# Kernel tuning notes

Measured on AMD Instinct MI355X. Metric: run time of the kernel, lower is better.

The kernel has to match this reference:

```python
import jax, jax.numpy as jnp
import numpy as np
import math

D_MODEL = 1024
N_HEADS = 16
D_K = D_MODEL // N_HEADS
HIDDEN = 4096
R_SOFTPLUS_0 = 1.442695041
EPS = 1e-6


def setup_inputs() -> dict:
    key = jax.random.key(0)
    ks = jax.random.split(key, 16)
    B, S = 4, 2048
    s = 0.02
    inp = {
        "inputs": jax.random.normal(ks[0], (B, S, D_MODEL), jnp.float32),
        "mask": jnp.zeros((1, 1, S, S), jnp.float32),
        # RmsNorm (direct_scale=True -> init 1.0)
        "rms_scale": jnp.ones((D_MODEL,), jnp.float32),
        # attention projections (torch Linear: y = x @ W.T + b)
        "Wq": jax.random.normal(ks[1], (D_MODEL, D_MODEL), jnp.float32) * s,
        "bq": jnp.zeros((D_MODEL,), jnp.float32),
        "Wk": jax.random.normal(ks[2], (D_MODEL, D_MODEL), jnp.float32) * s,
        "bk": jnp.zeros((D_MODEL,), jnp.float32),
        "Wv": jax.random.normal(ks[3], (D_MODEL, D_MODEL), jnp.float32) * s,
        "bv": jnp.zeros((D_MODEL,), jnp.float32),
        "per_dim_scale": jnp.zeros((D_K,), jnp.float32),
        "Wpost": jax.random.normal(ks[4], (D_MODEL, D_MODEL), jnp.float32) * s,
        "bpost": jnp.zeros((D_MODEL,), jnp.float32),
        # FFN LayerNorm (direct_scale=False -> scale param init 0, effective 1+scale)
        "ln_scale": jnp.zeros((D_MODEL,), jnp.float32),
        "ln_bias": jnp.zeros((D_MODEL,), jnp.float32),
        "W1": jax.random.normal(ks[5], (HIDDEN, D_MODEL), jnp.float32) * s,
        "b1": jnp.zeros((HIDDEN,), jnp.float32),
        "W2": jax.random.normal(ks[6], (D_MODEL, HIDDEN), jnp.float32) * s,
        "b2": jnp.zeros((D_MODEL,), jnp.float32),
    }
    return inp


def _rms_norm(x, scale):
    ms = jnp.mean(x * x, axis=-1, keepdims=True)
    return x * jax.lax.rsqrt(ms + EPS) * scale


def _layer_norm(x, scale, bias):
    mean = jnp.mean(x, axis=-1, keepdims=True)
    var = jnp.mean((x - mean) ** 2, axis=-1, keepdims=True)
    return (x - mean) * jax.lax.rsqrt(var + EPS) * (1.0 + scale) + bias


def reference(inputs, mask, rms_scale, Wq, bq, Wk, bk, Wv, bv, per_dim_scale,
              Wpost, bpost, ln_scale, ln_bias, W1, b1, W2, b2):
    B, S, _ = inputs.shape
    x = _rms_norm(inputs, rms_scale)
    # projections -> [B, H, S, Dk]
    def split_heads(t):
        return t.reshape(B, S, N_HEADS, D_K).transpose(0, 2, 1, 3)
    q = split_heads(x @ Wq.T + bq)
    k = split_heads(x @ Wk.T + bk)
    v = split_heads(x @ Wv.T + bv)
    # PerDimScale: (r_softplus_0 / sqrt(d_k)) * softplus(param)
    scale = (R_SOFTPLUS_0 / math.sqrt(D_K)) * jax.nn.softplus(per_dim_scale)
    q = q * scale
    attn = jnp.einsum("bhqd,bhkd->bhqk", q, k) + mask
    attn = jax.nn.softmax(attn, axis=-1)
    out = jnp.einsum("bhqk,bhkd->bhqd", attn, v)
    out = out.transpose(0, 2, 1, 3).reshape(B, S, D_MODEL)
    attn_out = out @ Wpost.T + bpost
    h = attn_out + inputs  # residual (dropout=0)
    # FeedForward with pre-LayerNorm and residual
    y = _layer_norm(h, ln_scale, ln_bias)
    y = jax.nn.relu(y @ W1.T + b1)
    y = y @ W2.T + b2
    return y + h
```

## Files before the change

kernel.cpp:

```cpp
#include <hip/hip_runtime.h>
#include <hip/hip_bf16.h>

typedef unsigned short u16;
typedef __attribute__((ext_vector_type(8))) short short8;
typedef __attribute__((ext_vector_type(4))) float floatx4;

#define R_PDS 0.18033688f
#define LOG2E 1.4426950408889634f

__device__ __forceinline__ float bf2f(u16 u) {
    union { float f; unsigned int i; } c; c.i = ((unsigned int)u) << 16; return c.f;
}
__device__ __forceinline__ u16 f2b(float f) {
    union { float f; unsigned int i; } c; c.f = f;
    unsigned int r = c.i + 0x7fffu + ((c.i >> 16) & 1u);
    return (u16)(r >> 16);
}
__device__ __forceinline__ unsigned int pk2(float a, float b) {
    __hip_bfloat162 h = __float22bfloat162_rn(float2{a, b});
    unsigned int u; __builtin_memcpy(&u, &h, 4); return u;
}

__device__ __forceinline__ void async16(const u16* g, u16* l) {
    __builtin_amdgcn_global_load_lds(
        (const __attribute__((address_space(1))) unsigned int*)g,
        (__attribute__((address_space(3))) unsigned int*)l, 16, 0, 0);
}

__global__ __launch_bounds__(256) void f2b_all_k(const float* __restrict__ Wq, const float* __restrict__ Wk,
                                                 const float* __restrict__ Wv, const float* __restrict__ Wp,
                                                 const float* __restrict__ W1, const float* __restrict__ W2,
                                                 u16* __restrict__ Wqkvb, u16* __restrict__ Wpb,
                                                 u16* __restrict__ W1b,  u16* __restrict__ W2b,
                                                 int* flag) {
    int bid = blockIdx.x;
    if (bid == 0 && threadIdx.x == 0) *flag = 0;
    const float* src; u16* dst; int off;
    if      (bid < 1024) { src = Wq; dst = Wqkvb;                off = bid; }
    else if (bid < 2048) { src = Wk; dst = Wqkvb + 1024 * 1024;  off = bid - 1024; }
    else if (bid < 3072) { src = Wv; dst = Wqkvb + 2048 * 1024;  off = bid - 2048; }
    else if (bid < 4096) { src = Wp; dst = Wpb;                  off = bid - 3072; }
    else if (bid < 8192) { src = W1; dst = W1b;                  off = bid - 4096; }
    else                 { src = W2; dst = W2b;                  off = bid - 8192; }
    int i = off * 256 + threadIdx.x;
    float4 v = ((const float4*)src)[i];
    uint2 w; w.x = pk2(v.x, v.y); w.y = pk2(v.z, v.w);
    ((uint2*)dst)[i] = w;
}

__global__ __launch_bounds__(256) void mask_any_k(const float* __restrict__ mask, int* flag) {
    int i = blockIdx.x * 256 + threadIdx.x;
    uint4 u = ((const uint4*)mask)[i];
    unsigned int v = (u.x | u.y | u.z | u.w) & 0x7fffffffu;
    if (v) atomicOr(flag, 1);
}

__global__ __launch_bounds__(256) void rmsnorm_k(const float* __restrict__ in,
                                                 const float* __restrict__ gscale,
                                                 u16* __restrict__ out) {
    int row = blockIdx.x;
    int t = threadIdx.x, lane = t & 63, wave = t >> 6;
    const float* x = in + (size_t)row * 1024;
    float4 v = *(const float4*)(x + t * 4);
    float ss = v.x*v.x + v.y*v.y + v.z*v.z + v.w*v.w;
    for (int o = 1; o < 64; o <<= 1) ss += __shfl_xor(ss, o, 64);
    __shared__ float red[4];
    if (lane == 0) red[wave] = ss;
    __syncthreads();
    float tot = red[0] + red[1] + red[2] + red[3];
    float inv = rsqrtf(tot * (1.0f / 1024.0f) + 1e-6f);
    float4 s = *(const float4*)(gscale + t * 4);
    uint2 w;
    w.x = pk2(v.x * inv * s.x, v.y * inv * s.y);
    w.y = pk2(v.z * inv * s.z, v.w * inv * s.w);
    *(uint2*)(out + (size_t)row * 1024 + t * 4) = w;
}

__global__ __launch_bounds__(256) void layernorm_k(const u16* __restrict__ in,
                                                   const float* __restrict__ gs,
                                                   const float* __restrict__ gb,
                                                   u16* __restrict__ out) {
    int row = blockIdx.x;
    int t = threadIdx.x, lane = t & 63, wave = t >> 6;
    const u16* x = in + (size_t)row * 1024;
    uint2 u = *(const uint2*)(x + t * 4);
    float v0 = bf2f((u16)(u.x & 0xffff)), v1 = bf2f((u16)(u.x >> 16));
    float v2 = bf2f((u16)(u.y & 0xffff)), v3 = bf2f((u16)(u.y >> 16));
    float s1 = v0 + v1 + v2 + v3;
    float s2 = v0*v0 + v1*v1 + v2*v2 + v3*v3;
    for (int o = 1; o < 64; o <<= 1) { s1 += __shfl_xor(s1, o, 64); s2 += __shfl_xor(s2, o, 64); }
    __shared__ float r1[4], r2[4];
    if (lane == 0) { r1[wave] = s1; r2[wave] = s2; }
    __syncthreads();
    float mean = (r1[0] + r1[1] + r1[2] + r1[3]) * (1.0f / 1024.0f);
    float var  = (r2[0] + r2[1] + r2[2] + r2[3]) * (1.0f / 1024.0f) - mean * mean;
    var = fmaxf(var, 0.0f);
    float inv = rsqrtf(var + 1e-6f);
    float4 sc = *(const float4*)(gs + t * 4);
    float4 bb = *(const float4*)(gb + t * 4);
    uint2 w;
    w.x = pk2((v0 - mean) * inv * (1.0f + sc.x) + bb.x,
              (v1 - mean) * inv * (1.0f + sc.y) + bb.y);
    w.y = pk2((v2 - mean) * inv * (1.0f + sc.z) + bb.z,
              (v3 - mean) * inv * (1.0f + sc.w) + bb.w);
    *(uint2*)(out + (size_t)row * 1024 + t * 4) = w;
}

__device__ __forceinline__ void xcd_swizzle(int& bx, int& by) {
    int gx = gridDim.x, nwg = gx * gridDim.y;
    int lin = blockIdx.y * gx + blockIdx.x;
    int swz = (lin & 7) * (nwg >> 3) + (lin >> 3);
    bx = swz % gx; by = swz / gx;
}

__device__ __forceinline__ void gemm8_core(const u16* __restrict__ A, const u16* __restrict__ B,
                                           int K, int NG, int m0, int n0,
                                           u16* lds, floatx4 (&acc)[8][4]) {
    const int t = threadIdx.x, wave = t >> 6, lane = t & 63;
    const int quad = lane >> 4, ln = lane & 15;
    const int wave_m = wave >> 2, wave_n = wave & 3;

    const int rowS = t >> 3;
    const int srcb = ((t & 7) * 16) ^ (((t >> 3) & 7) << 4);
    const u16* Ab = A + (size_t)(m0 + rowS) * K + (srcb >> 1);
    const u16* Bb = B + (size_t)(n0 + rowS) * K + (srcb >> 1);
    const size_t rstep = (size_t)64 * K;
    const size_t hstep = (size_t)128 * K;
    const int ldw = wave * 512;

    #define STAGE_A8(buf, h, kt) do { \
        u16* _l = lds + (buf) * 32768 + (h) * 8192 + ldw; \
        const u16* _g = Ab + (size_t)(h) * hstep + (kt); \
        async16(_g, _l); async16(_g + rstep, _l + 4096); } while (0)
    #define STAGE_B8(buf, h, kt) do { \
        u16* _l = lds + (buf) * 32768 + 16384 + (h) * 8192 + ldw; \
        const u16* _g = Bb + (size_t)(h) * hstep + (kt); \
        async16(_g, _l); async16(_g + rstep, _l + 4096); } while (0)

    #define RD8(base, lr, ks) \
        (*(const short8*)((base) + (lr) * 64 + ((((ks) * 64 + quad * 16) ^ (((lr) & 7) << 4)) >> 1)))

    STAGE_B8(0, 0, 0); STAGE_B8(0, 1, 0);
    STAGE_A8(0, 0, 0); STAGE_A8(0, 1, 0);
    if (NG > 1) {
        STAGE_B8(1, 0, 64); STAGE_B8(1, 1, 64);
        asm volatile("s_waitcnt vmcnt(4)" ::: "memory");
    } else {
        asm volatile("s_waitcnt vmcnt(0)" ::: "memory");
    }
    __builtin_amdgcn_s_barrier();

    for (int g = 0; g < NG; ++g) {
        const int cur = g & 1;
        const u16* aH = lds + cur * 32768 + wave_m * 8192;
        const u16* bH = lds + cur * 32768 + 16384 + (wave_n >> 1) * 8192;
        const int lrB = (wave_n & 1) * 64;
        short8 bf[4][2];
        #pragma unroll
        for (int q = 0; q < 4; ++q) {
            short8 af[2][2];
            #pragma unroll
            for (int mt = 0; mt < 2; ++mt)
                #pragma unroll
                for (int ks = 0; ks < 2; ++ks)
                    af[mt][ks] = RD8(aH, q * 32 + mt * 16 + ln, ks);
            if (q == 0) {
                #pragma unroll
                for (int nt = 0; nt < 4; ++nt)
                    #pragma unroll
                    for (int ks = 0; ks < 2; ++ks)
                        bf[nt][ks] = RD8(bH, lrB + nt * 16 + ln, ks);
            }
            if (q == 0 && g + 1 < NG) STAGE_A8(cur ^ 1, 0, (g + 1) * 64);
            if (q == 1 && g + 1 < NG) STAGE_A8(cur ^ 1, 1, (g + 1) * 64);
            if (q == 2 && g + 2 < NG) STAGE_B8(cur, 0, (g + 2) * 64);
            if (q == 3 && g + 2 < NG) STAGE_B8(cur, 1, (g + 2) * 64);
            __builtin_amdgcn_s_barrier();
            asm volatile("s_waitcnt lgkmcnt(0)" ::: "memory");
            __builtin_amdgcn_sched_barrier(0);
            __builtin_amdgcn_s_setprio(1);
            #pragma unroll
            for (int ks = 0; ks < 2; ++ks)
                #pragma unroll
                for (int mt = 0; mt < 2; ++mt)
                    #pragma unroll
                    for (int nt = 0; nt < 4; ++nt)
                        acc[q * 2 + mt][nt] = __builtin_amdgcn_mfma_f32_16x16x32_bf16(
                            af[mt][ks], bf[nt][ks], acc[q * 2 + mt][nt], 0, 0, 0);
            __builtin_amdgcn_s_setprio(0);
            __builtin_amdgcn_sched_barrier(0);
            if (q == 3 && g + 1 < NG) {
                if (g + 2 < NG) asm volatile("s_waitcnt vmcnt(4)" ::: "memory");
                else            asm volatile("s_waitcnt vmcnt(0)" ::: "memory");
            }
            __builtin_amdgcn_s_barrier();
        }
    }
    #undef STAGE_A8
    #undef STAGE_B8
    #undef RD8
}

__device__ __forceinline__ void gemm8h_core(const u16* __restrict__ A, const u16* __restrict__ B,
                                            int K, int NG, int m0, int n0,
                                            u16* lds, floatx4 (&acc)[4][4]) {
    const int t = threadIdx.x, wave = t >> 6, lane = t & 63;
    const int quad = lane >> 4, ln = lane & 15;
    const int wm = (wave >> 2) * 64, wn = (wave & 3) * 64;

    const int rowS = t >> 3;
    const int srcb = ((t & 7) * 16) ^ (((t >> 3) & 7) << 4);
    const u16* Ab = A + (size_t)(m0 + rowS) * K + (srcb >> 1);
    const u16* Bb = B + (size_t)(n0 + rowS) * K + (srcb >> 1);
    const size_t hstep = (size_t)64 * K;
    const int ldw = wave * 512;

    #define STAGE_AH(buf, h, kt) \
        async16(Ab + (size_t)(h) * hstep + (kt), lds + (buf) * 24576 + (h) * 4096 + ldw)
    #define STAGE_BH(buf, h, kt) \
        async16(Bb + (size_t)(h) * hstep + (kt), lds + (buf) * 24576 + 8192 + (h) * 4096 + ldw)
    #define RD8H(base, lr, ks) \
        (*(const short8*)((base) + (lr) * 64 + ((((ks) * 64 + quad * 16) ^ (((lr) & 7) << 4)) >> 1)))

    STAGE_BH(0, 0, 0); STAGE_BH(0, 1, 0); STAGE_BH(0, 2, 0); STAGE_BH(0, 3, 0);
    STAGE_AH(0, 0, 0); STAGE_AH(0, 1, 0);
    if (NG > 1) {
        STAGE_BH(1, 0, 64); STAGE_BH(1, 1, 64); STAGE_BH(1, 2, 64); STAGE_BH(1, 3, 64);
        asm volatile("s_waitcnt vmcnt(4)" ::: "memory");
    } else {
        asm volatile("s_waitcnt vmcnt(0)" ::: "memory");
    }
    __builtin_amdgcn_s_barrier();

    for (int g = 0; g < NG; ++g) {
        const int cur = g & 1;
        const u16* aB = lds + cur * 24576;
        const u16* bB = lds + cur * 24576 + 8192;
        short8 bf[4][2];
        #pragma unroll
        for (int q = 0; q < 2; ++q) {
            short8 af[2][2];
            #pragma unroll
            for (int mt = 0; mt < 2; ++mt)
                #pragma unroll
                for (int ks = 0; ks < 2; ++ks)
                    af[mt][ks] = RD8H(aB, wm + (q * 2 + mt) * 16 + ln, ks);
            if (q == 0) {
                #pragma unroll
                for (int nt = 0; nt < 4; ++nt)
                    #pragma unroll
                    for (int ks = 0; ks < 2; ++ks)
                        bf[nt][ks] = RD8H(bB, wn + nt * 16 + ln, ks);
            }
            if (q == 0 && g + 1 < NG) {
                STAGE_AH(cur ^ 1, 0, (g + 1) * 64); STAGE_AH(cur ^ 1, 1, (g + 1) * 64);
            }
            if (q == 1 && g + 2 < NG) {
                STAGE_BH(cur, 0, (g + 2) * 64); STAGE_BH(cur, 1, (g + 2) * 64);
                STAGE_BH(cur, 2, (g + 2) * 64); STAGE_BH(cur, 3, (g + 2) * 64);
            }
            __builtin_amdgcn_s_barrier();
            asm volatile("s_waitcnt lgkmcnt(0)" ::: "memory");
            __builtin_amdgcn_sched_barrier(0);
            __builtin_amdgcn_s_setprio(1);
            #pragma unroll
            for (int ks = 0; ks < 2; ++ks)
                #pragma unroll
                for (int mt = 0; mt < 2; ++mt)
                    #pragma unroll
                    for (int nt = 0; nt < 4; ++nt)
                        acc[q * 2 + mt][nt] = __builtin_amdgcn_mfma_f32_16x16x32_bf16(
                            af[mt][ks], bf[nt][ks], acc[q * 2 + mt][nt], 0, 0, 0);
            __builtin_amdgcn_s_setprio(0);
            __builtin_amdgcn_sched_barrier(0);
            if (q == 1 && g + 1 < NG) {
                if (g + 2 < NG) asm volatile("s_waitcnt vmcnt(4)" ::: "memory");
                else            asm volatile("s_waitcnt vmcnt(0)" ::: "memory");
            }
            __builtin_amdgcn_s_barrier();
        }
    }
    #undef STAGE_AH
    #undef STAGE_BH
    #undef RD8H
}

template <int EPI, bool OUTF32, bool RESF32>
__global__ __launch_bounds__(512, 2) void gemm8_bt_k(const u16* __restrict__ A,
                                                     const u16* __restrict__ B,
                                                     const float* __restrict__ bias,
                                                     const void* __restrict__ res,
                                                     void* __restrict__ Cv,
                                                     int M, int N, int K) {
    __shared__ __align__(16) u16 lds[65536];
    int bx, by; xcd_swizzle(bx, by);
    const int m0 = by * 256, n0 = bx * 256;
    const int t = threadIdx.x, wave = t >> 6, lane = t & 63;
    const int quad = lane >> 4, ln = lane & 15;
    const int wm = (wave >> 2) * 128, wn = (wave & 3) * 64;

    floatx4 acc[8][4];
    #pragma unroll
    for (int mf = 0; mf < 8; mf++)
        #pragma unroll
        for (int nf = 0; nf < 4; nf++) acc[mf][nf] = (floatx4)0.0f;

    gemm8_core(A, B, K, K >> 6, m0, n0, lds, acc);

    #pragma unroll
    for (int nf = 0; nf < 4; nf++) {
        int col = n0 + wn + nf * 16 + ln;
        float bv = bias[col];
        #pragma unroll
        for (int mf = 0; mf < 8; mf++) {
            int row = m0 + wm + mf * 16 + quad * 4;
            #pragma unroll
            for (int r = 0; r < 4; r++) {
                float v = acc[mf][nf][r] + bv;
                if (EPI == 1) v = fmaxf(v, 0.0f);
                if (EPI == 2) {
                    if (RESF32) v += ((const float*)res)[(size_t)(row + r) * N + col];
                    else        v += bf2f(((const u16*)res)[(size_t)(row + r) * N + col]);
                }
                if (OUTF32) ((float*)Cv)[(size_t)(row + r) * N + col] = v;
                else        ((u16*)Cv)[(size_t)(row + r) * N + col] = f2b(v);
            }
        }
    }
}

template <int EPI, bool OUTF32, bool RESF32>
__global__ __launch_bounds__(512, 2) void gemm8h_bt_k(const u16* __restrict__ A,
                                                      const u16* __restrict__ B,
                                                      const float* __restrict__ bias,
                                                      const void* __restrict__ res,
                                                      void* __restrict__ Cv,
                                                      int M, int N, int K) {
    __shared__ __align__(16) u16 lds[49152];
    int bx, by; xcd_swizzle(bx, by);
    const int m0 = by * 128, n0 = bx * 256;
    const int t = threadIdx.x, wave = t >> 6, lane = t & 63;
    const int quad = lane >> 4, ln = lane & 15;
    const int wm = (wave >> 2) * 64, wn = (wave & 3) * 64;

    floatx4 acc[4][4];
    #pragma unroll
    for (int mf = 0; mf < 4; mf++)
        #pragma unroll
        for (int nf = 0; nf < 4; nf++) acc[mf][nf] = (floatx4)0.0f;

    gemm8h_core(A, B, K, K >> 6, m0, n0, lds, acc);

    #pragma unroll
    for (int nf = 0; nf < 4; nf++) {
        int col = n0 + wn + nf * 16 + ln;
        float bv = bias[col];
        #pragma unroll
        for (int mf = 0; mf < 4; mf++) {
            int row = m0 + wm + mf * 16 + quad * 4;
            #pragma unroll
            for (int r = 0; r < 4; r++) {
                float v = acc[mf][nf][r] + bv;
                if (EPI == 1) v = fmaxf(v, 0.0f);
                if (EPI == 2) {
                    if (RESF32) v += ((const float*)res)[(size_t)(row + r) * N + col];
                    else        v += bf2f(((const u16*)res)[(size_t)(row + r) * N + col]);
                }
                if (OUTF32) ((float*)Cv)[(size_t)(row + r) * N + col] = v;
                else        ((u16*)Cv)[(size_t)(row + r) * N + col] = f2b(v);
            }
        }
    }
}

__global__ __launch_bounds__(512, 2) void gemm8h_qkv_k(const u16* __restrict__ A,
                                                       const u16* __restrict__ B,
                                                       const float* __restrict__ bq,
                                                       const float* __restrict__ bk,
                                                       const float* __restrict__ bv,
                                                       const float* __restrict__ pds,
                                                       u16* __restrict__ C) {
    const int K = 1024, N = 3072;
    __shared__ __align__(16) u16 lds[49152];
    int bx, by; xcd_swizzle(bx, by);
    const int m0 = by * 128, n0 = bx * 256;
    const int t = threadIdx.x, wave = t >> 6, lane = t & 63;
    const int quad = lane >> 4, ln = lane & 15;
    const int wm = (wave >> 2) * 64, wn = (wave & 3) * 64;

    floatx4 acc[4][4];
    #pragma unroll
    for (int mf = 0; mf < 4; mf++)
        #pragma unroll
        for (int nf = 0; nf < 4; nf++) acc[mf][nf] = (floatx4)0.0f;

    gemm8h_core(A, B, K, K >> 6, m0, n0, lds, acc);

    #pragma unroll
    for (int nf = 0; nf < 4; nf++) {
        int col = n0 + wn + nf * 16 + ln;
        float bv_, sc = 1.0f;
        if (col < 1024) {
            bv_ = bq[col];
            float xp = pds[col & 63];
            float sp = (xp > 20.0f) ? xp : log1pf(__expf(xp));
            sc = R_PDS * sp * LOG2E;
        } else if (col < 2048) bv_ = bk[col - 1024];
        else                   bv_ = bv[col - 2048];
        #pragma unroll
        for (int mf = 0; mf < 4; mf++) {
            int row = m0 + wm + mf * 16 + quad * 4;
            #pragma unroll
            for (int r = 0; r < 4; r++)
                C[(size_t)(row + r) * N + col] = f2b((acc[mf][nf][r] + bv_) * sc);
        }
    }
}

__global__ __launch_bounds__(256) void transpose_v_k(const u16* __restrict__ qkv, u16* __restrict__ vT) {
    __shared__ u16 tile[64][65];
    int st = blockIdx.x, bh = blockIdx.y;
    int b = bh >> 4, h = bh & 15;
    const u16* vb = qkv + (size_t)(b * 2048 + st * 64) * 3072 + 2048 + h * 64;
    int t = threadIdx.x;
    for (int i = t; i < 4096; i += 256) {
        int s = i >> 6, d = i & 63;
        tile[s][d] = vb[(size_t)s * 3072 + d];
    }
    __syncthreads();
    u16* ob = vT + (size_t)bh * 131072 + st * 64;
    for (int i = t; i < 4096; i += 256) {
        int d = i >> 6, s = i & 63;
        ob[(size_t)d * 2048 + s] = tile[s][d];
    }
}

__global__ __launch_bounds__(256) void attn_k(const u16* __restrict__ qkv,
                                              const u16* __restrict__ vT,
                                              const float* __restrict__ mask,
                                              const int* __restrict__ flag,
                                              u16* __restrict__ o) {
    __shared__ __align__(16) u16 QPs[128][72];
    __shared__ __align__(16) u16 Ks[64][72];
    __shared__ __align__(16) u16 Vs[64][72];

    const int t = threadIdx.x, wave = t >> 6, lane = t & 63;
    const int quad = lane >> 4, ln = lane & 15;
    const int qt = blockIdx.x, bh = blockIdx.y;
    const int b = bh >> 4, h = bh & 15;
    const int q0 = qt * 128;
    const int wm = wave * 32;

    const u16* qb = qkv + (size_t)(b * 2048 + q0) * 3072 + h * 64;
    for (int c = t; c < 1024; c += 256) {
        int row = c >> 3, seg = c & 7;
        *(uint4*)&QPs[row][seg * 8] = *(const uint4*)(qb + (size_t)row * 3072 + seg * 8);
    }
    __syncthreads();

    short8 qf[2][2];
    for (int mt = 0; mt < 2; mt++)
        for (int ks = 0; ks < 2; ks++)
            qf[mt][ks] = *(const short8*)&QPs[wm + mt * 16 + ln][ks * 32 + quad * 8];

    short8 ones_f;
    for (int i = 0; i < 8; i++) ones_f[i] = (short)0x3F80;

    floatx4 acc_o[2][4], acc_l[2];
    for (int mt = 0; mt < 2; mt++) {
        acc_l[mt] = (floatx4)0.0f;
        for (int dt = 0; dt < 4; dt++) acc_o[mt][dt] = (floatx4)0.0f;
    }

    const int mflag = *flag;
    const u16* kb = qkv + (size_t)(b * 2048) * 3072 + 1024 + h * 64;
    const u16* vg = vT + (size_t)bh * 131072;

    const int r0 = t >> 3, s0 = (t & 7) * 8;
    const u16* kp0 = kb + (size_t)r0 * 3072 + s0;
    const u16* kp1 = kb + (size_t)(r0 + 32) * 3072 + s0;
    const u16* vp0 = vg + (size_t)r0 * 2048 + s0;
    const u16* vp1 = vg + (size_t)(r0 + 32) * 2048 + s0;

    uint4 kr0 = *(const uint4*)(kp0);
    uint4 kr1 = *(const uint4*)(kp1);
    uint4 vr0 = *(const uint4*)(vp0);
    uint4 vr1 = *(const uint4*)(vp1);

    for (int kv0 = 0; kv0 < 2048; kv0 += 64) {
        __syncthreads();
        *(uint4*)&Ks[r0][s0]      = kr0;
        *(uint4*)&Ks[r0 + 32][s0] = kr1;
        *(uint4*)&Vs[r0][s0]      = vr0;
        *(uint4*)&Vs[r0 + 32][s0] = vr1;
        __syncthreads();
        if (kv0 + 64 < 2048) {
            size_t ko = (size_t)(kv0 + 64) * 3072;
            int    vo = kv0 + 64;
            kr0 = *(const uint4*)(kp0 + ko);
            kr1 = *(const uint4*)(kp1 + ko);
            vr0 = *(const uint4*)(vp0 + vo);
            vr1 = *(const uint4*)(vp1 + vo);
        }

        for (int nt = 0; nt < 4; nt++) {
            floatx4 sa0 = (floatx4)0.0f, sa1 = (floatx4)0.0f;
            for (int ks = 0; ks < 2; ks++) {
                short8 kf = *(const short8*)&Ks[nt * 16 + ln][ks * 32 + quad * 8];
                sa0 = __builtin_amdgcn_mfma_f32_16x16x32_bf16(kf, qf[0][ks], sa0, 0, 0, 0);
                sa1 = __builtin_amdgcn_mfma_f32_16x16x32_bf16(kf, qf[1][ks], sa1, 0, 0, 0);
            }
            if (mflag) {
                for (int r = 0; r < 4; r++) {
                    int kc = kv0 + nt * 16 + quad * 4 + r;
                    sa0[r] += mask[(size_t)(q0 + wm + ln) * 2048 + kc] * LOG2E;
                    sa1[r] += mask[(size_t)(q0 + wm + 16 + ln) * 2048 + kc] * LOG2E;
                }
            }
            {
                uint2 w;
                w.x = pk2(__builtin_amdgcn_exp2f(fminf(sa0[0], 80.0f)),
                          __builtin_amdgcn_exp2f(fminf(sa0[1], 80.0f)));
                w.y = pk2(__builtin_amdgcn_exp2f(fminf(sa0[2], 80.0f)),
                          __builtin_amdgcn_exp2f(fminf(sa0[3], 80.0f)));
                *(uint2*)&QPs[wm + ln][nt * 16 + quad * 4] = w;
            }
            {
                uint2 w;
                w.x = pk2(__builtin_amdgcn_exp2f(fminf(sa1[0], 80.0f)),
                          __builtin_amdgcn_exp2f(fminf(sa1[1], 80.0f)));
                w.y = pk2(__builtin_amdgcn_exp2f(fminf(sa1[2], 80.0f)),
                          __builtin_amdgcn_exp2f(fminf(sa1[3], 80.0f)));
                *(uint2*)&QPs[wm + 16 + ln][nt * 16 + quad * 4] = w;
            }
        }

        for (int ks = 0; ks < 2; ks++) {
            short8 a0 = *(const short8*)&QPs[wm + ln][ks * 32 + quad * 8];
            short8 a1 = *(const short8*)&QPs[wm + 16 + ln][ks * 32 + quad * 8];
            acc_l[0] = __builtin_amdgcn_mfma_f32_16x16x32_bf16(a0, ones_f, acc_l[0], 0, 0, 0);
            acc_l[1] = __builtin_amdgcn_mfma_f32_16x16x32_bf16(a1, ones_f, acc_l[1], 0, 0, 0);
            for (int dt = 0; dt < 4; dt++) {
                short8 bfr = *(const short8*)&Vs[dt * 16 + ln][ks * 32 + quad * 8];
                acc_o[0][dt] = __builtin_amdgcn_mfma_f32_16x16x32_bf16(a0, bfr, acc_o[0][dt], 0, 0, 0);
                acc_o[1][dt] = __builtin_amdgcn_mfma_f32_16x16x32_bf16(a1, bfr, acc_o[1][dt], 0, 0, 0);
            }
        }
    }

    u16* ob = o + (size_t)(b * 2048 + q0) * 1024 + h * 64;
    for (int mt = 0; mt < 2; mt++) {
        for (int r = 0; r < 4; r++) {
            float inv = 1.0f / acc_l[mt][r];
            int row = wm + mt * 16 + quad * 4 + r;
            for (int dt = 0; dt < 4; dt++)
                ob[(size_t)row * 1024 + dt * 16 + ln] = f2b(acc_o[mt][dt][r] * inv);
        }
    }
}

extern "C" void kernel_launch(void* const* d_in, const int* in_sizes, int n_in,
                              void* d_out, int out_size, void* d_ws, size_t ws_size,
                              hipStream_t stream) {
    const float* inp    = (const float*)d_in[0];
    const float* mask   = (const float*)d_in[1];
    const float* rms_s  = (const float*)d_in[2];
    const float* Wq     = (const float*)d_in[3];
    const float* bq     = (const float*)d_in[4];
    const float* Wk     = (const float*)d_in[5];
    const float* bk     = (const float*)d_in[6];
    const float* Wv     = (const float*)d_in[7];
    const float* bv     = (const float*)d_in[8];
    const float* pds    = (const float*)d_in[9];
    const float* Wpost  = (const float*)d_in[10];
    const float* bpost  = (const float*)d_in[11];
    const float* ln_s   = (const float*)d_in[12];
    const float* ln_b   = (const float*)d_in[13];
    const float* W1     = (const float*)d_in[14];
    const float* b1     = (const float*)d_in[15];
    const float* W2     = (const float*)d_in[16];
    const float* b2     = (const float*)d_in[17];
    float* out = (float*)d_out;

    char* w = (char*)d_ws;
    const size_t MB = 1u << 20;
    u16* W1b   = (u16*)(w + 0 * MB);
    u16* W2b   = (u16*)(w + 8 * MB);
    u16* qkv   = (u16*)(w + 16 * MB);
    u16* x     = (u16*)(w + 64 * MB);
    u16* o     = (u16*)(w + 64 * MB);
    u16* Wqkvb = (u16*)(w + 80 * MB);
    u16* Wpb   = (u16*)(w + 86 * MB);
    u16* yln   = (u16*)(w + 80 * MB);
    u16* vT    = (u16*)(w + 96 * MB);
    u16* hb    = (u16*)(w + 96 * MB);
    u16* f1    = (u16*)(w + 16 * MB);
    int* flag  = (int*)(w + 112 * MB);

    f2b_all_k<<<12288, 256, 0, stream>>>(Wq, Wk, Wv, Wpost, W1, W2, Wqkvb, Wpb, W1b, W2b, flag);
    mask_any_k<<<4096, 256, 0, stream>>>(mask, flag);

    rmsnorm_k<<<8192, 256, 0, stream>>>(inp, rms_s, x);

    gemm8h_qkv_k<<<dim3(12, 64), 512, 0, stream>>>(x, Wqkvb, bq, bk, bv, pds, qkv);

    transpose_v_k<<<dim3(32, 64), 256, 0, stream>>>(qkv, vT);

    attn_k<<<dim3(16, 64), 256, 0, stream>>>(qkv, vT, mask, flag, o);

    gemm8h_bt_k<2, false, true><<<dim3(4, 64), 512, 0, stream>>>(o, Wpb, bpost, inp, hb, 8192, 1024, 1024);

    layernorm_k<<<8192, 256, 0, stream>>>(hb, ln_s, ln_b, yln);

    gemm8_bt_k<1, false, true><<<dim3(16, 32), 512, 0, stream>>>(yln, W1b, b1, nullptr, f1, 8192, 4096, 1024);
    gemm8h_bt_k<2, true, false><<<dim3(4, 64), 512, 0, stream>>>(f1, W2b, b2, hb, out, 8192, 1024, 4096);
}
```

Baseline: 556.9 us.

## Enlarge attention query tile to 256 rows with swizzled LDS and remapped blocks

The attention kernel now processes 256 query rows per block instead of 128, with each wave owning four 16-row M tiles. Each K/V tile loaded into LDS therefore feeds twice as many MFMAs. LDS padding is replaced by an XOR swizzle to avoid bank conflicts with denser storage. Block indices are remapped so neighbouring blocks share a head, for L2 locality. The cost is more accumulator registers (launch bounds ask for 2 blocks per SM) and half as many blocks, which may lower occupancy.

Measured after the change: 506.2 us. -9.1%, faster.

```diff
diff --git a/kernel.cpp b/kernel.cpp
--- a/kernel.cpp
+++ b/kernel.cpp
@@ -435,40 +435,53 @@
     }
 }
 
-__global__ __launch_bounds__(256) void attn_k(const u16* __restrict__ qkv,
-                                              const u16* __restrict__ vT,
-                                              const float* __restrict__ mask,
-                                              const int* __restrict__ flag,
-                                              u16* __restrict__ o) {
-    __shared__ __align__(16) u16 QPs[128][72];
-    __shared__ __align__(16) u16 Ks[64][72];
-    __shared__ __align__(16) u16 Vs[64][72];
+__global__ __launch_bounds__(256, 2) void attn_k(const u16* __restrict__ qkv,
+                                                 const u16* __restrict__ vT,
+                                                 const float* __restrict__ mask,
+                                                 const int* __restrict__ flag,
+                                                 u16* __restrict__ o) {
+    __shared__ __align__(16) u16 QPs[256 * 64];
+    __shared__ __align__(16) u16 Ks[64 * 64];
+    __shared__ __align__(16) u16 Vs[64 * 64];
 
     const int t = threadIdx.x, wave = t >> 6, lane = t & 63;
     const int quad = lane >> 4, ln = lane & 15;
-    const int qt = blockIdx.x, bh = blockIdx.y;
+    const int lin = blockIdx.y * 8 + blockIdx.x;
+    const int qt = (lin >> 3) & 7;
+    const int bh = ((lin & 7) << 3) | (lin >> 6);
     const int b = bh >> 4, h = bh & 15;
-    const int q0 = qt * 128;
-    const int wm = wave * 32;
+    const int q0 = qt * 256;
+    const int wm = wave * 64;
 
     const u16* qb = qkv + (size_t)(b * 2048 + q0) * 3072 + h * 64;
-    for (int c = t; c < 1024; c += 256) {
+    #pragma unroll
+    for (int i = 0; i < 8; i++) {
+        int c = t + i * 256;
         int row = c >> 3, seg = c & 7;
-        *(uint4*)&QPs[row][seg * 8] = *(const uint4*)(qb + (size_t)row * 3072 + seg * 8);
+        int byt = (seg * 16) ^ ((row & 7) << 4);
+        *(uint4*)&QPs[row * 64 + (byt >> 1)] = *(const uint4*)(qb + (size_t)row * 3072 + seg * 8);
     }
     __syncthreads();
 
-    short8 qf[2][2];
-    for (int mt = 0; mt < 2; mt++)
-        for (int ks = 0; ks < 2; ks++)
-            qf[mt][ks] = *(const short8*)&QPs[wm + mt * 16 + ln][ks * 32 + quad * 8];
+    short8 qf[4][2];
+    #pragma unroll
+    for (int mt = 0; mt < 4; mt++)
+        #pragma unroll
+        for (int ks = 0; ks < 2; ks++) {
+            int row = wm + mt * 16 + ln;
+            int byt = (ks * 64 + quad * 16) ^ ((ln & 7) << 4);
+            qf[mt][ks] = *(const short8*)&QPs[row * 64 + (byt >> 1)];
+        }
 
     short8 ones_f;
+    #pragma unroll
     for (int i = 0; i < 8; i++) ones_f[i] = (short)0x3F80;
 
-    floatx4 acc_o[2][4], acc_l[2];
-    for (int mt = 0; mt < 2; mt++) {
+    floatx4 acc_o[4][4], acc_l[4];
+    #pragma unroll
+    for (int mt = 0; mt < 4; mt++) {
         acc_l[mt] = (floatx4)0.0f;
+        #pragma unroll
         for (int dt = 0; dt < 4; dt++) acc_o[mt][dt] = (floatx4)0.0f;
     }
 
@@ -476,7 +489,9 @@
     const u16* kb = qkv + (size_t)(b * 2048) * 3072 + 1024 + h * 64;
     const u16* vg = vT + (size_t)bh * 131072;
 
-    const int r0 = t >> 3, s0 = (t & 7) * 8;
+    const int r0 = t >> 3, sseg = t & 7;
+    const int wofs = (((sseg * 16) ^ ((r0 & 7) << 4)) >> 1);
+    const int s0 = sseg * 8;
     const u16* kp0 = kb + (size_t)r0 * 3072 + s0;
     const u16* kp1 = kb + (size_t)(r0 + 32) * 3072 + s0;
     const u16* vp0 = vg + (size_t)r0 * 2048 + s0;
@@ -489,10 +504,10 @@
 
     for (int kv0 = 0; kv0 < 2048; kv0 += 64) {
         __syncthreads();
-        *(uint4*)&Ks[r0][s0]      = kr0;
-        *(uint4*)&Ks[r0 + 32][s0] = kr1;
-        *(uint4*)&Vs[r0][s0]      = vr0;
-        *(uint4*)&Vs[r0 + 32][s0] = vr1;
+        *(uint4*)&Ks[r0 * 64 + wofs]        = kr0;
+        *(uint4*)&Ks[(r0 + 32) * 64 + wofs] = kr1;
+        *(uint4*)&Vs[r0 * 64 + wofs]        = vr0;
+        *(uint4*)&Vs[(r0 + 32) * 64 + wofs] = vr1;
         __syncthreads();
         if (kv0 + 64 < 2048) {
             size_t ko = (size_t)(kv0 + 64) * 3072;
@@ -503,56 +518,72 @@
             vr1 = *(const uint4*)(vp1 + vo);
         }
 
+        #pragma unroll
         for (int nt = 0; nt < 4; nt++) {
-            floatx4 sa0 = (floatx4)0.0f, sa1 = (floatx4)0.0f;
+            floatx4 sa[4];
+            #pragma unroll
+            for (int mt = 0; mt < 4; mt++) sa[mt] = (floatx4)0.0f;
+            #pragma unroll
             for (int ks = 0; ks < 2; ks++) {
-                short8 kf = *(const short8*)&Ks[nt * 16 + ln][ks * 32 + quad * 8];
-                sa0 = __builtin_amdgcn_mfma_f32_16x16x32_bf16(kf, qf[0][ks], sa0, 0, 0, 0);
-                sa1 = __builtin_amdgcn_mfma_f32_16x16x32_bf16(kf, qf[1][ks], sa1, 0, 0, 0);
+                int byt = (ks * 64 + quad * 16) ^ ((ln & 7) << 4);
+                short8 kf = *(const short8*)&Ks[(nt * 16 + ln) * 64 + (byt >> 1)];
+                #pragma unroll
+                for (int mt = 0; mt < 4; mt++)
+                    sa[mt] = __builtin_amdgcn_mfma_f32_16x16x32_bf16(kf, qf[mt][ks], sa[mt], 0, 0, 0);
             }
             if (mflag) {
-                for (int r = 0; r < 4; r++) {
-                    int kc = kv0 + nt * 16 + quad * 4 + r;
-                    sa0[r] += mask[(size_t)(q0 + wm + ln) * 2048 + kc] * LOG2E;
-                    sa1[r] += mask[(size_t)(q0 + wm + 16 + ln) * 2048 + kc] * LOG2E;
-                }
-            }
-            {
+                #pragma unroll
+                for (int mt = 0; mt < 4; mt++)
+                    #pragma unroll
+                    for (int r = 0; r < 4; r++) {
+                        int kc = kv0 + nt * 16 + quad * 4 + r;
+                        sa[mt][r] += mask[(size_t)(q0 + wm + mt * 16 + ln) * 2048 + kc] * LOG2E;
+                    }
+            }
+            #pragma unroll
+            for (int mt = 0; mt < 4; mt++) {
                 uint2 w;
-                w.x = pk2(__builtin_amdgcn_exp2f(fminf(sa0[0], 80.0f)),
-                          __builtin_amdgcn_exp2f(fminf(sa0[1], 80.0f)));
-                w.y = pk2(__builtin_amdgcn_exp2f(fminf(sa0[2], 80.0f)),
-                          __builtin_amdgcn_exp2f(fminf(sa0[3], 80.0f)));
-                *(uint2*)&QPs[wm + ln][nt * 16 + quad * 4] = w;
-            }
-            {
-                uint2 w;
-                w.x = pk2(__builtin_amdgcn_exp2f(fminf(sa1[0], 80.0f)),
-                          __builtin_amdgcn_exp2f(fminf(sa1[1], 80.0f)));
-                w.y = pk2(__builtin_amdgcn_exp2f(fminf(sa1[2], 80.0f)),
-                          __builtin_amdgcn_exp2f(fminf(sa1[3], 80.0f)));
-                *(uint2*)&QPs[wm + 16 + ln][nt * 16 + quad * 4] = w;
-            }
-        }
-
+                w.x = pk2(__builtin_amdgcn_exp2f(fminf(sa[mt][0], 80.0f)),
+                          __builtin_amdgcn_exp2f(fminf(sa[mt][1], 80.0f)));
+                w.y = pk2(__builtin_amdgcn_exp2f(fminf(sa[mt][2], 80.0f)),
+                          __builtin_amdgcn_exp2f(fminf(sa[mt][3], 80.0f)));
+                int row = wm + mt * 16 + ln;
+                int byt = (nt * 32 + quad * 8) ^ ((ln & 7) << 4);
+                *(uint2*)&QPs[row * 64 + (byt >> 1)] = w;
+            }
+        }
+
+        #pragma unroll
         for (int ks = 0; ks < 2; ks++) {
-            short8 a0 = *(const short8*)&QPs[wm + ln][ks * 32 + quad * 8];
-            short8 a1 = *(const short8*)&QPs[wm + 16 + ln][ks * 32 + quad * 8];
-            acc_l[0] = __builtin_amdgcn_mfma_f32_16x16x32_bf16(a0, ones_f, acc_l[0], 0, 0, 0);
-            acc_l[1] = __builtin_amdgcn_mfma_f32_16x16x32_bf16(a1, ones_f, acc_l[1], 0, 0, 0);
+            short8 a[4];
+            #pragma unroll
+            for (int mt = 0; mt < 4; mt++) {
+                int row = wm + mt * 16 + ln;
+                int byt = (ks * 64 + quad * 16) ^ ((ln & 7) << 4);
+                a[mt] = *(const short8*)&QPs[row * 64 + (byt >> 1)];
+            }
+            #pragma unroll
+            for (int mt = 0; mt < 4; mt++)
+                acc_l[mt] = __builtin_amdgcn_mfma_f32_16x16x32_bf16(a[mt], ones_f, acc_l[mt], 0, 0, 0);
+            #pragma unroll
             for (int dt = 0; dt < 4; dt++) {
-                short8 bfr = *(const short8*)&Vs[dt * 16 + ln][ks * 32 + quad * 8];
-                acc_o[0][dt] = __builtin_amdgcn_mfma_f32_16x16x32_bf16(a0, bfr, acc_o[0][dt], 0, 0, 0);
-                acc_o[1][dt] = __builtin_amdgcn_mfma_f32_16x16x32_bf16(a1, bfr, acc_o[1][dt], 0, 0, 0);
+                int byt = (ks * 64 + quad * 16) ^ ((ln & 7) << 4);
+                short8 bfr = *(const short8*)&Vs[(dt * 16 + ln) * 64 + (byt >> 1)];
+                #pragma unroll
+                for (int mt = 0; mt < 4; mt++)
+                    acc_o[mt][dt] = __builtin_amdgcn_mfma_f32_16x16x32_bf16(a[mt], bfr, acc_o[mt][dt], 0, 0, 0);
             }
         }
     }
 
     u16* ob = o + (size_t)(b * 2048 + q0) * 1024 + h * 64;
-    for (int mt = 0; mt < 2; mt++) {
+    #pragma unroll
+    for (int mt = 0; mt < 4; mt++) {
+        #pragma unroll
         for (int r = 0; r < 4; r++) {
             float inv = 1.0f / acc_l[mt][r];
             int row = wm + mt * 16 + quad * 4 + r;
+            #pragma unroll
             for (int dt = 0; dt < 4; dt++)
                 ob[(size_t)row * 1024 + dt * 16 + ln] = f2b(acc_o[mt][dt][r] * inv);
         }
@@ -606,7 +637,7 @@
 
     transpose_v_k<<<dim3(32, 64), 256, 0, stream>>>(qkv, vT);
 
-    attn_k<<<dim3(16, 64), 256, 0, stream>>>(qkv, vT, mask, flag, o);
+    attn_k<<<dim3(8, 64), 256, 0, stream>>>(qkv, vT, mask, flag, o);
 
     gemm8h_bt_k<2, false, true><<<dim3(4, 64), 512, 0, stream>>>(o, Wpb, bpost, inp, hb, 8192, 1024, 1024);
 
```

## Restructure attention kernel with async LDS double-buffering and swizzled smem

Applied to the files above, without the earlier changes.

Rewrites the attention inner loop to stream K and V tiles of 32 keys straight into LDS with async global-to-LDS loads, double-buffered so the next tile loads while the current one is computed. It adds XOR swizzling to the K, V and P shared-memory layouts to avoid bank conflicts, loads Q fragments directly from global memory, remaps block indices to group heads for L2 reuse, and sets occupancy via launch bounds. The cost is more barriers per key tile because tiles are smaller, and hand-written vmcnt waits that must match the number of loads in flight.

After: 518.7 us. 6.9% less time.

```diff
diff --git a/kernel.cpp b/kernel.cpp
--- a/kernel.cpp
+++ b/kernel.cpp
@@ -435,124 +435,162 @@
     }
 }
 
-__global__ __launch_bounds__(256) void attn_k(const u16* __restrict__ qkv,
-                                              const u16* __restrict__ vT,
-                                              const float* __restrict__ mask,
-                                              const int* __restrict__ flag,
-                                              u16* __restrict__ o) {
-    __shared__ __align__(16) u16 QPs[128][72];
-    __shared__ __align__(16) u16 Ks[64][72];
-    __shared__ __align__(16) u16 Vs[64][72];
+__global__ __launch_bounds__(256, 4) void attn_k(const u16* __restrict__ qkv,
+                                                 const u16* __restrict__ vT,
+                                                 const float* __restrict__ mask,
+                                                 const int* __restrict__ flag,
+                                                 u16* __restrict__ o) {
+    __shared__ __align__(16) u16 Ksh[4096];
+    __shared__ __align__(16) u16 Vsh[4096];
+    __shared__ __align__(16) u16 Ps[4096];
 
     const int t = threadIdx.x, wave = t >> 6, lane = t & 63;
     const int quad = lane >> 4, ln = lane & 15;
-    const int qt = blockIdx.x, bh = blockIdx.y;
+    const int lin = blockIdx.y * 16 + blockIdx.x;
+    const int qt = (lin >> 3) & 15;
+    const int bh = ((lin & 7) << 3) | (lin >> 7);
     const int b = bh >> 4, h = bh & 15;
     const int q0 = qt * 128;
     const int wm = wave * 32;
 
     const u16* qb = qkv + (size_t)(b * 2048 + q0) * 3072 + h * 64;
-    for (int c = t; c < 1024; c += 256) {
-        int row = c >> 3, seg = c & 7;
-        *(uint4*)&QPs[row][seg * 8] = *(const uint4*)(qb + (size_t)row * 3072 + seg * 8);
-    }
-    __syncthreads();
-
     short8 qf[2][2];
+    #pragma unroll
     for (int mt = 0; mt < 2; mt++)
+        #pragma unroll
         for (int ks = 0; ks < 2; ks++)
-            qf[mt][ks] = *(const short8*)&QPs[wm + mt * 16 + ln][ks * 32 + quad * 8];
+            qf[mt][ks] = *(const short8*)(qb + (size_t)(wm + mt * 16 + ln) * 3072 + ks * 32 + quad * 8);
+
+    const int swzK = (ln & 7) << 4;
+    const int swzP = (ln & 3) << 4;
+    const int o_kA0 = ln * 128 + ((quad * 16) ^ swzK);
+    const int o_kA1 = ln * 128 + ((64 + quad * 16) ^ swzK);
+    const int o_pv  = ln * 64 + ((quad * 16) ^ swzP);
+    const int o_pw0 = wave * 2048 + ln * 64 + ((quad * 8) ^ swzP);
+    const int o_pw1 = wave * 2048 + ln * 64 + ((32 + quad * 8) ^ swzP);
+    const int o_pr  = wave * 2048 + o_pv;
+
+    #define RD8AT(arr, byteoff) (*(const short8*)((const char*)(arr) + (byteoff)))
+
+    const int rK = t >> 3, sK = (((t & 7) ^ (rK & 7))) * 8;
+    const int rV = t >> 2, sV = (((t & 3) ^ (rV & 3))) * 8;
+    const u16* kgp = qkv + (size_t)(b * 2048) * 3072 + 1024 + h * 64 + (size_t)rK * 3072 + sK;
+    const u16* vgp = vT + (size_t)bh * 131072 + (size_t)rV * 2048 + sV;
+    const size_t KADV = (size_t)32 * 3072;
+
+    #define STAGE(c, tile) do { \
+        async16(kgp + (size_t)(tile) * KADV, Ksh + (c) * 2048 + t * 8); \
+        async16(vgp + (size_t)(tile) * 32,   Vsh + (c) * 2048 + t * 8); } while (0)
 
     short8 ones_f;
+    #pragma unroll
     for (int i = 0; i < 8; i++) ones_f[i] = (short)0x3F80;
 
     floatx4 acc_o[2][4], acc_l[2];
+    #pragma unroll
     for (int mt = 0; mt < 2; mt++) {
         acc_l[mt] = (floatx4)0.0f;
+        #pragma unroll
         for (int dt = 0; dt < 4; dt++) acc_o[mt][dt] = (floatx4)0.0f;
     }
 
     const int mflag = *flag;
-    const u16* kb = qkv + (size_t)(b * 2048) * 3072 + 1024 + h * 64;
-    const u16* vg = vT + (size_t)bh * 131072;
-
-    const int r0 = t >> 3, s0 = (t & 7) * 8;
-    const u16* kp0 = kb + (size_t)r0 * 3072 + s0;
-    const u16* kp1 = kb + (size_t)(r0 + 32) * 3072 + s0;
-    const u16* vp0 = vg + (size_t)r0 * 2048 + s0;
-    const u16* vp1 = vg + (size_t)(r0 + 32) * 2048 + s0;
-
-    uint4 kr0 = *(const uint4*)(kp0);
-    uint4 kr1 = *(const uint4*)(kp1);
-    uint4 vr0 = *(const uint4*)(vp0);
-    uint4 vr1 = *(const uint4*)(vp1);
-
-    for (int kv0 = 0; kv0 < 2048; kv0 += 64) {
-        __syncthreads();
-        *(uint4*)&Ks[r0][s0]      = kr0;
-        *(uint4*)&Ks[r0 + 32][s0] = kr1;
-        *(uint4*)&Vs[r0][s0]      = vr0;
-        *(uint4*)&Vs[r0 + 32][s0] = vr1;
-        __syncthreads();
-        if (kv0 + 64 < 2048) {
-            size_t ko = (size_t)(kv0 + 64) * 3072;
-            int    vo = kv0 + 64;
-            kr0 = *(const uint4*)(kp0 + ko);
-            kr1 = *(const uint4*)(kp1 + ko);
-            vr0 = *(const uint4*)(vp0 + vo);
-            vr1 = *(const uint4*)(vp1 + vo);
-        }
-
-        for (int nt = 0; nt < 4; nt++) {
-            floatx4 sa0 = (floatx4)0.0f, sa1 = (floatx4)0.0f;
-            for (int ks = 0; ks < 2; ks++) {
-                short8 kf = *(const short8*)&Ks[nt * 16 + ln][ks * 32 + quad * 8];
-                sa0 = __builtin_amdgcn_mfma_f32_16x16x32_bf16(kf, qf[0][ks], sa0, 0, 0, 0);
-                sa1 = __builtin_amdgcn_mfma_f32_16x16x32_bf16(kf, qf[1][ks], sa1, 0, 0, 0);
-            }
-            if (mflag) {
-                for (int r = 0; r < 4; r++) {
-                    int kc = kv0 + nt * 16 + quad * 4 + r;
-                    sa0[r] += mask[(size_t)(q0 + wm + ln) * 2048 + kc] * LOG2E;
-                    sa1[r] += mask[(size_t)(q0 + wm + 16 + ln) * 2048 + kc] * LOG2E;
-                }
-            }
-            {
-                uint2 w;
-                w.x = pk2(__builtin_amdgcn_exp2f(fminf(sa0[0], 80.0f)),
-                          __builtin_amdgcn_exp2f(fminf(sa0[1], 80.0f)));
-                w.y = pk2(__builtin_amdgcn_exp2f(fminf(sa0[2], 80.0f)),
-                          __builtin_amdgcn_exp2f(fminf(sa0[3], 80.0f)));
-                *(uint2*)&QPs[wm + ln][nt * 16 + quad * 4] = w;
-            }
-            {
-                uint2 w;
-                w.x = pk2(__builtin_amdgcn_exp2f(fminf(sa1[0], 80.0f)),
-                          __builtin_amdgcn_exp2f(fminf(sa1[1], 80.0f)));
-                w.y = pk2(__builtin_amdgcn_exp2f(fminf(sa1[2], 80.0f)),
-                          __builtin_amdgcn_exp2f(fminf(sa1[3], 80.0f)));
-                *(uint2*)&QPs[wm + 16 + ln][nt * 16 + quad * 4] = w;
-            }
-        }
-
-        for (int ks = 0; ks < 2; ks++) {
-            short8 a0 = *(const short8*)&QPs[wm + ln][ks * 32 + quad * 8];
-            short8 a1 = *(const short8*)&QPs[wm + 16 + ln][ks * 32 + quad * 8];
-            acc_l[0] = __builtin_amdgcn_mfma_f32_16x16x32_bf16(a0, ones_f, acc_l[0], 0, 0, 0);
-            acc_l[1] = __builtin_amdgcn_mfma_f32_16x16x32_bf16(a1, ones_f, acc_l[1], 0, 0, 0);
-            for (int dt = 0; dt < 4; dt++) {
-                short8 bfr = *(const short8*)&Vs[dt * 16 + ln][ks * 32 + quad * 8];
-                acc_o[0][dt] = __builtin_amdgcn_mfma_f32_16x16x32_bf16(a0, bfr, acc_o[0][dt], 0, 0, 0);
-                acc_o[1][dt] = __builtin_amdgcn_mfma_f32_16x16x32_bf16(a1, bfr, acc_o[1][dt], 0, 0, 0);
-            }
-        }
-    }
+    int kvbase = 0;
+
+    STAGE(0, 0);
+    STAGE(1, 1);
+    asm volatile("s_waitcnt vmcnt(2)" ::: "memory");
+    __builtin_amdgcn_s_barrier();
+
+    #define COMPUTE(BUF) do {                                                              \
+                           \
+        _Pragma("unroll")                                                                  \
+        for (int nt = 0; nt < 2; nt++) {                                                   \
+            short8 kf0 = RD8AT(Ksh, (BUF) * 4096 + nt * 2048 + o_kA0);                     \
+            short8 kf1 = RD8AT(Ksh, (BUF) * 4096 + nt * 2048 + o_kA1);                     \
+            floatx4 sa0 = (floatx4)0.0f, sa1 = (floatx4)0.0f;                              \
+            sa0 = __builtin_amdgcn_mfma_f32_16x16x32_bf16(kf0, qf[0][0], sa0, 0, 0, 0);    \
+            sa0 = __builtin_amdgcn_mfma_f32_16x16x32_bf16(kf1, qf[0][1], sa0, 0, 0, 0);    \
+            sa1 = __builtin_amdgcn_mfma_f32_16x16x32_bf16(kf0, qf[1][0], sa1, 0, 0, 0);    \
+            sa1 = __builtin_amdgcn_mfma_f32_16x16x32_bf16(kf1, qf[1][1], sa1, 0, 0, 0);    \
+            if (mflag) {                                                                   \
+                _Pragma("unroll")                                                          \
+                for (int r = 0; r < 4; r++) {                                              \
+                    int kc = kvbase + nt * 16 + quad * 4 + r;                              \
+                    sa0[r] += mask[(size_t)(q0 + wm + ln) * 2048 + kc] * LOG2E;            \
+                    sa1[r] += mask[(size_t)(q0 + wm + 16 + ln) * 2048 + kc] * LOG2E;       \
+                }                                                                          \
+            }                                                                              \
+            {                                                                              \
+                uint2 w;                                                                   \
+                w.x = pk2(__builtin_amdgcn_exp2f(fminf(sa0[0], 80.0f)),                    \
+                          __builtin_amdgcn_exp2f(fminf(sa0[1], 80.0f)));                   \
+                w.y = pk2(__builtin_amdgcn_exp2f(fminf(sa0[2], 80.0f)),                    \
+                          __builtin_amdgcn_exp2f(fminf(sa0[3], 80.0f)));                   \
+                *(uint2*)((char*)Ps + (nt ? o_pw1 : o_pw0)) = w;                           \
+            }                                                                              \
+            {                                                                              \
+                uint2 w;                                                                   \
+                w.x = pk2(__builtin_amdgcn_exp2f(fminf(sa1[0], 80.0f)),                    \
+                          __builtin_amdgcn_exp2f(fminf(sa1[1], 80.0f)));                   \
+                w.y = pk2(__builtin_amdgcn_exp2f(fminf(sa1[2], 80.0f)),                    \
+                          __builtin_amdgcn_exp2f(fminf(sa1[3], 80.0f)));                   \
+                *(uint2*)((char*)Ps + (nt ? o_pw1 : o_pw0) + 1024) = w;                    \
+            }                                                                              \
+        }                                                                                  \
+                                     \
+        {                                                                                  \
+            short8 vf0 = RD8AT(Vsh, (BUF) * 4096 + 0 * 1024 + o_pv);                       \
+            short8 vf1 = RD8AT(Vsh, (BUF) * 4096 + 1 * 1024 + o_pv);                       \
+            short8 vf2 = RD8AT(Vsh, (BUF) * 4096 + 2 * 1024 + o_pv);                       \
+            short8 vf3 = RD8AT(Vsh, (BUF) * 4096 + 3 * 1024 + o_pv);                       \
+            _Pragma("unroll")                                                              \
+            for (int mt = 0; mt < 2; mt++) {                                               \
+                short8 a = RD8AT(Ps, o_pr + mt * 1024);                                    \
+                acc_l[mt] = __builtin_amdgcn_mfma_f32_16x16x32_bf16(a, ones_f, acc_l[mt], 0, 0, 0); \
+                acc_o[mt][0] = __builtin_amdgcn_mfma_f32_16x16x32_bf16(a, vf0, acc_o[mt][0], 0, 0, 0); \
+                acc_o[mt][1] = __builtin_amdgcn_mfma_f32_16x16x32_bf16(a, vf1, acc_o[mt][1], 0, 0, 0); \
+                acc_o[mt][2] = __builtin_amdgcn_mfma_f32_16x16x32_bf16(a, vf2, acc_o[mt][2], 0, 0, 0); \
+                acc_o[mt][3] = __builtin_amdgcn_mfma_f32_16x16x32_bf16(a, vf3, acc_o[mt][3], 0, 0, 0); \
+            }                                                                              \
+        }                                                                                  \
+    } while (0)
+
+    #pragma unroll 1
+    for (int it = 0; it < 32; ++it) {
+        COMPUTE(0);
+        __builtin_amdgcn_s_barrier();
+        if (it < 31) {
+            STAGE(0, 2 * it + 2);
+            asm volatile("s_waitcnt vmcnt(2)" ::: "memory");
+        } else {
+            asm volatile("s_waitcnt vmcnt(0)" ::: "memory");
+        }
+        __builtin_amdgcn_s_barrier();
+        kvbase += 32;
+        COMPUTE(1);
+        __builtin_amdgcn_s_barrier();
+        if (it < 31) {
+            STAGE(1, 2 * it + 3);
+            asm volatile("s_waitcnt vmcnt(2)" ::: "memory");
+        } else {
+            asm volatile("s_waitcnt vmcnt(0)" ::: "memory");
+        }
+        __builtin_amdgcn_s_barrier();
+        kvbase += 32;
+    }
+    #undef COMPUTE
+    #undef STAGE
+    #undef RD8AT
 
     u16* ob = o + (size_t)(b * 2048 + q0) * 1024 + h * 64;
+    #pragma unroll
     for (int mt = 0; mt < 2; mt++) {
+        #pragma unroll
         for (int r = 0; r < 4; r++) {
             float inv = 1.0f / acc_l[mt][r];
             int row = wm + mt * 16 + quad * 4 + r;
+            #pragma unroll
             for (int dt = 0; dt < 4; dt++)
                 ob[(size_t)row * 1024 + dt * 16 + ln] = f2b(acc_o[mt][dt][r] * inv);
         }
```
